# Optimization experiments

Measured on AMD Instinct MI355X. Metric: run time of the kernel, lower is better.

## Reference

```python
import jax, jax.numpy as jnp
import numpy as np

B, T, D, H, Dh, DF, MH = 4, 1024, 1024, 16, 64, 4096, 256
EPS = 1e-6


def setup_inputs() -> dict:
    key = jax.random.key(0)
    ks = jax.random.split(key, 10)
    s = 0.02
    w = lambda k, shape: jax.random.normal(k, shape, jnp.float32) * s
    return {
        "x": jax.random.normal(ks[0], (B, T, D), jnp.float32),
        "norm1_w": jnp.ones((D,), jnp.float32),
        "norm2_w": jnp.ones((D,), jnp.float32),
        "wq": w(ks[1], (D, D)),
        "wk": w(ks[2], (D, D)),
        "wv": w(ks[3], (D, D)),
        "wo": w(ks[4], (D, D)),
        "mnet_w1": w(ks[5], (D, MH)),
        "mnet_w2": w(ks[6], (MH, H * Dh)),
        "gate_w": w(ks[7], (D, DF)),
        "up_w": w(ks[8], (D, DF)),
        "down_w": w(ks[9], (DF, D)),
    }


def _rmsnorm(x, w):
    rms = jnp.sqrt(jnp.mean(x * x, axis=-1, keepdims=True) + EPS)
    return w * (x / rms)


def reference(x, norm1_w, norm2_w, wq, wk, wv, wo, mnet_w1, mnet_w2, gate_w, up_w, down_w):
    # --- pre-norm geodesic (DRM) attention ---
    h = _rmsnorm(x, norm1_w)  # [B,T,D]
    q = (h @ wq).reshape(B, T, H, Dh)
    k = (h @ wk).reshape(B, T, H, Dh)
    v = (h @ wv).reshape(B, T, H, Dh)
    # MetricNet: positive diagonal metric G(x) per token/head
    g = jax.nn.softplus(jax.nn.silu(h @ mnet_w1) @ mnet_w2).reshape(B, T, H, Dh)
    # squared geodesic distance under key-side diagonal metric, expanded form:
    # dist_ij = sum_d g_jd*(q_id - k_jd)^2 = q^2.g - 2 q.(g*k) + sum(g*k^2)
    gk = g * k
    dist = (
        jnp.einsum("bihd,bjhd->bhij", q * q, g)
        - 2.0 * jnp.einsum("bihd,bjhd->bhij", q, gk)
        + jnp.transpose(jnp.sum(gk * k, axis=-1), (0, 2, 1))[:, :, None, :]
    )  # [B,H,T,T]
    scores = -dist / np.float32(np.sqrt(Dh))
    causal = jnp.tril(jnp.ones((T, T), bool))
    scores = jnp.where(causal, scores, jnp.float32(-1e30))
    attn = jax.nn.softmax(scores, axis=-1)
    o = jnp.einsum("bhij,bjhd->bihd", attn, v).reshape(B, T, D) @ wo
    x = x + o
    # --- pre-norm SwiGLU FFN ---
    h2 = _rmsnorm(x, norm2_w)
    ffn = (jax.nn.silu(h2 @ gate_w) * (h2 @ up_w)) @ down_w
    return x + ffn
```

## Files before the change

### kernel.cpp

```cpp
#include <hip/hip_runtime.h>
#include <hip/hip_bf16.h>
#include <math.h>

#define BB  4
#define TT  1024
#define DD  1024
#define HH  16
#define DH  64
#define DFF 4096
#define MHH 256

typedef __attribute__((ext_vector_type(8))) short bf16x8;
typedef __attribute__((ext_vector_type(4))) float f32x4;
typedef unsigned int u32;

#define NEG_BIG (-1e9f)

__device__ __forceinline__ float b2f(short s) {
    union { unsigned int u; float f; } x;
    x.u = ((unsigned int)(unsigned short)s) << 16;
    return x.f;
}
__device__ __forceinline__ short f2b(float f) {
    union { float f; unsigned int u; } x; x.f = f;
    unsigned int r = x.u + 0x7fffu + ((x.u >> 16) & 1u);
    return (short)(r >> 16);
}
__device__ __forceinline__ float silu_f(float x) { return x / (1.f + __expf(-x)); }

__device__ __forceinline__ void gld16(const short* g, short* l) {
    __builtin_amdgcn_global_load_lds(
        (const __attribute__((address_space(1))) u32*)g,
        (__attribute__((address_space(3))) u32*)l, 16, 0, 0);
}

#define STAGE64(ga0, ga1, lds, kb)                                  \
    {                                                               \
        gld16((ga0) + (kb),      &(lds)[tid * 8]);                  \
        gld16((ga1) + (kb),      &(lds)[2048 + tid * 8]);           \
        gld16((ga0) + (kb) + 32, &(lds)[4096 + tid * 8]);           \
        gld16((ga1) + (kb) + 32, &(lds)[4096 + 2048 + tid * 8]);    \
    }

__device__ __forceinline__ void convT_tile_body(
    const float* __restrict__ src, short* __restrict__ dst,
    int K, int N, int bx, int by, int tid, short (*Ts)[36])
{
    const int k0 = by * 32, n0 = bx * 32;
    const int r = tid >> 3, c4 = (tid & 7) * 4;
    float4 v = *(const float4*)(src + (size_t)(k0 + r) * N + n0 + c4);
    Ts[r][c4 + 0] = f2b(v.x); Ts[r][c4 + 1] = f2b(v.y);
    Ts[r][c4 + 2] = f2b(v.z); Ts[r][c4 + 3] = f2b(v.w);
    __syncthreads();
    short4 o;
    o.x = Ts[c4 + 0][r]; o.y = Ts[c4 + 1][r];
    o.z = Ts[c4 + 2][r]; o.w = Ts[c4 + 3][r];
    *(short4*)(dst + (size_t)(n0 + r) * K + k0 + c4) = o;
}

__device__ __forceinline__ void rms_body(
    const float* __restrict__ X, const float* __restrict__ W,
    short* __restrict__ O, float* __restrict__ XC, int row, int tid, float* red)
{
    float4 xv = ((const float4*)(X + (size_t)row * DD))[tid];
    if (XC) ((float4*)(XC + (size_t)row * DD))[tid] = xv;
    float f0 = xv.x, f1 = xv.y, f2 = xv.z, f3 = xv.w;
    float ss = f0*f0 + f1*f1 + f2*f2 + f3*f3;
    #pragma unroll
    for (int m = 1; m < 64; m <<= 1) ss += __shfl_xor(ss, m);
    if ((tid & 63) == 0) red[tid >> 6] = ss;
    __syncthreads();
    float tot = red[0] + red[1] + red[2] + red[3];
    float scale = rsqrtf(tot * (1.f / DD) + 1e-6f);
    float4 wv = ((const float4*)W)[tid];
    short4 ov;
    ov.x = f2b(f0 * scale * wv.x);
    ov.y = f2b(f1 * scale * wv.y);
    ov.z = f2b(f2 * scale * wv.z);
    ov.w = f2b(f3 * scale * wv.w);
    ((short4*)(O + (size_t)row * DD))[tid] = ov;
}

__global__ __launch_bounds__(256) void pre_k(
    const float* __restrict__ wq, const float* __restrict__ wk,
    const float* __restrict__ wv, const float* __restrict__ mw1,
    const float* __restrict__ wo, const float* __restrict__ mw2,
    short* __restrict__ WfT, short* __restrict__ woT, short* __restrict__ mw2T,
    const float* __restrict__ x, const float* __restrict__ n1w,
    short* __restrict__ h, float* __restrict__ out)
{
    __shared__ __align__(16) short Ts[32][36];
    __shared__ float red[4];
    const int b = blockIdx.x, tid = threadIdx.x;
    if (b >= 4608) { rms_body(x, n1w, h, out, b - 4608, tid, red); return; }
    const float* src; short* dst; int K, N, bx, by;
    if (b < 1024)      { src = wq;  dst = WfT;               K = DD;  N = DD;  int l = b;        bx = l & 31; by = l >> 5; }
    else if (b < 2048) { src = wk;  dst = WfT + 1024 * 1024; K = DD;  N = DD;  int l = b - 1024; bx = l & 31; by = l >> 5; }
    else if (b < 3072) { src = wv;  dst = WfT + 2048 * 1024; K = DD;  N = DD;  int l = b - 2048; bx = l & 31; by = l >> 5; }
    else if (b < 3328) { src = mw1; dst = WfT + 3072 * 1024; K = DD;  N = MHH; int l = b - 3072; bx = l & 7;  by = l >> 3; }
    else if (b < 4352) { src = wo;  dst = woT;               K = DD;  N = DD;  int l = b - 3328; bx = l & 31; by = l >> 5; }
    else               { src = mw2; dst = mw2T;              K = MHH; N = DD;  int l = b - 4352; bx = l & 31; by = l >> 5; }
    convT_tile_body(src, dst, K, N, bx, by, tid, Ts);
}

__global__ __launch_bounds__(256) void ffn_k(
    const float* __restrict__ gw, const float* __restrict__ uw,
    const float* __restrict__ dw,
    short* __restrict__ WgT, short* __restrict__ WuT, short* __restrict__ WdT,
    const float* __restrict__ out, const float* __restrict__ n2w,
    short* __restrict__ h2)
{
    __shared__ __align__(16) short Ts[32][36];
    __shared__ float red[4];
    const int b = blockIdx.x, tid = threadIdx.x;
    if (b >= 12288) { rms_body(out, n2w, h2, nullptr, b - 12288, tid, red); return; }
    const float* src; short* dst; int K, N, bx, by;
    if (b < 4096)      { src = gw; dst = WgT; K = DD;  N = DFF; int l = b;        bx = l & 127; by = l >> 7; }
    else if (b < 8192) { src = uw; dst = WuT; K = DD;  N = DFF; int l = b - 4096; bx = l & 127; by = l >> 7; }
    else               { src = dw; dst = WdT; K = DFF; N = DD;  int l = b - 8192; bx = l & 31;  by = l >> 5; }
    convT_tile_body(src, dst, K, N, bx, by, tid, Ts);
}

#define EP_NONE     0
#define EP_SILU     1
#define EP_SOFTPLUS 2
#define EP_RES      3

template<int EP, bool CF32, bool AUXF32>
__global__ __launch_bounds__(256, 4) void gemm128_k(
    const short* __restrict__ A, const short* __restrict__ Bt,
    void* Cv, const void* auxv,
    int N, int K, int lda, int ldb)
{
    __shared__ __align__(16) short As[2 * 4096];
    __shared__ __align__(16) short Bs[2 * 4096];
    const int tid  = threadIdx.x;
    const int wave = tid >> 6, lane = tid & 63;
    const int l16  = lane & 15, quad = lane >> 4;
    const int m0 = blockIdx.y * 128, n0 = blockIdx.x * 128;
    const int wm = (wave & 1) * 64, wn = (wave >> 1) * 64;

    f32x4 acc[4][4];
    #pragma unroll
    for (int i = 0; i < 4; i++)
        #pragma unroll
        for (int j = 0; j < 4; j++) acc[i][j] = (f32x4){0.f, 0.f, 0.f, 0.f};

    const int srow = tid >> 2, scol = (tid & 3) * 8;
    const short* ga0 = A  + (size_t)(m0 + srow)      * lda + scol;
    const short* ga1 = A  + (size_t)(m0 + 64 + srow) * lda + scol;
    const short* gb0 = Bt + (size_t)(n0 + srow)      * ldb + scol;
    const short* gb1 = Bt + (size_t)(n0 + 64 + srow) * ldb + scol;

    for (int kb = 0; kb < K; kb += 64) {
        STAGE64(ga0, ga1, As, kb);
        STAGE64(gb0, gb1, Bs, kb);
        __syncthreads();
        #pragma unroll
        for (int kc = 0; kc < 2; kc++) {
            bf16x8 af[4], bf[4];
            #pragma unroll
            for (int mi = 0; mi < 4; mi++)
                af[mi] = *(bf16x8*)&As[kc * 4096 + (wm + mi * 16 + l16) * 32 + quad * 8];
            #pragma unroll
            for (int ni = 0; ni < 4; ni++)
                bf[ni] = *(bf16x8*)&Bs[kc * 4096 + (wn + ni * 16 + l16) * 32 + quad * 8];
            #pragma unroll
            for (int mi = 0; mi < 4; mi++)
                #pragma unroll
                for (int ni = 0; ni < 4; ni++)
                    acc[mi][ni] = __builtin_amdgcn_mfma_f32_16x16x32_bf16(af[mi], bf[ni], acc[mi][ni], 0, 0, 0);
        }
        __syncthreads();
    }
    #pragma unroll
    for (int mi = 0; mi < 4; mi++) {
        #pragma unroll
        for (int ni = 0; ni < 4; ni++) {
            #pragma unroll
            for (int r = 0; r < 4; r++) {
                int row = m0 + wm + mi * 16 + quad * 4 + r;
                int col = n0 + wn + ni * 16 + l16;
                size_t idx = (size_t)row * N + col;
                float v = acc[mi][ni][r];
                if (EP == EP_SILU)          v = silu_f(v);
                else if (EP == EP_SOFTPLUS) v = fmaxf(v, 0.f) + log1pf(__expf(-fabsf(v)));
                else if (EP == EP_RES) {
                    if (AUXF32) v += ((const float*)auxv)[idx];
                    else        v += b2f(((const short*)auxv)[idx]);
                }
                if (CF32) ((float*)Cv)[idx] = v;
                else      ((short*)Cv)[idx] = f2b(v);
            }
        }
    }
}

__global__ __launch_bounds__(256, 4) void gemm128_atomic_k(
    const short* __restrict__ A, const short* __restrict__ Bt,
    float* out, int N, int Kc, int lda, int ldb)
{
    __shared__ __align__(16) short As[2 * 4096];
    __shared__ __align__(16) short Bs[2 * 4096];
    const int tid  = threadIdx.x;
    const int wave = tid >> 6, lane = tid & 63;
    const int l16  = lane & 15, quad = lane >> 4;
    const int m0 = blockIdx.y * 128, n0 = blockIdx.x * 128;
    const int wm = (wave & 1) * 64, wn = (wave >> 1) * 64;
    const int koff = blockIdx.z * Kc;

    f32x4 acc[4][4];
    #pragma unroll
    for (int i = 0; i < 4; i++)
        #pragma unroll
        for (int j = 0; j < 4; j++) acc[i][j] = (f32x4){0.f, 0.f, 0.f, 0.f};

    const int srow = tid >> 2, scol = (tid & 3) * 8;
    const short* ga0 = A  + (size_t)(m0 + srow)      * lda + koff + scol;
    const short* ga1 = A  + (size_t)(m0 + 64 + srow) * lda + koff + scol;
    const short* gb0 = Bt + (size_t)(n0 + srow)      * ldb + koff + scol;
    const short* gb1 = Bt + (size_t)(n0 + 64 + srow) * ldb + koff + scol;

    for (int kb = 0; kb < Kc; kb += 64) {
        STAGE64(ga0, ga1, As, kb);
        STAGE64(gb0, gb1, Bs, kb);
        __syncthreads();
        #pragma unroll
        for (int kc = 0; kc < 2; kc++) {
            bf16x8 af[4], bf[4];
            #pragma unroll
            for (int mi = 0; mi < 4; mi++)
                af[mi] = *(bf16x8*)&As[kc * 4096 + (wm + mi * 16 + l16) * 32 + quad * 8];
            #pragma unroll
            for (int ni = 0; ni < 4; ni++)
                bf[ni] = *(bf16x8*)&Bs[kc * 4096 + (wn + ni * 16 + l16) * 32 + quad * 8];
            #pragma unroll
            for (int mi = 0; mi < 4; mi++)
                #pragma unroll
                for (int ni = 0; ni < 4; ni++)
                    acc[mi][ni] = __builtin_amdgcn_mfma_f32_16x16x32_bf16(af[mi], bf[ni], acc[mi][ni], 0, 0, 0);
        }
        __syncthreads();
    }
    #pragma unroll
    for (int mi = 0; mi < 4; mi++)
        #pragma unroll
        for (int ni = 0; ni < 4; ni++)
            #pragma unroll
            for (int r = 0; r < 4; r++) {
                int row = m0 + wm + mi * 16 + quad * 4 + r;
                int col = n0 + wn + ni * 16 + l16;
                atomicAdd(out + (size_t)row * N + col, acc[mi][ni][r]);
            }
}

__global__ __launch_bounds__(256, 4) void gemm128_qkvm_k(
    const short* __restrict__ A, const short* __restrict__ Wf,
    short* __restrict__ Qb, short* __restrict__ Kb, short* __restrict__ Vb,
    short* __restrict__ M1)
{
    __shared__ __align__(16) short As[2 * 4096];
    __shared__ __align__(16) short Bs[2 * 4096];
    const int tid  = threadIdx.x;
    const int wave = tid >> 6, lane = tid & 63;
    const int l16  = lane & 15, quad = lane >> 4;
    const int m0 = blockIdx.y * 128, n0 = blockIdx.x * 128;
    const int wm = (wave & 1) * 64, wn = (wave >> 1) * 64;
    const int K = DD;

    f32x4 acc[4][4];
    #pragma unroll
    for (int i = 0; i < 4; i++)
        #pragma unroll
        for (int j = 0; j < 4; j++) acc[i][j] = (f32x4){0.f, 0.f, 0.f, 0.f};

    const int srow = tid >> 2, scol = (tid & 3) * 8;
    const short* ga0 = A  + (size_t)(m0 + srow)      * K + scol;
    const short* ga1 = A  + (size_t)(m0 + 64 + srow) * K + scol;
    const short* gb0 = Wf + (size_t)(n0 + srow)      * K + scol;
    const short* gb1 = Wf + (size_t)(n0 + 64 + srow) * K + scol;

    for (int kb = 0; kb < K; kb += 64) {
        STAGE64(ga0, ga1, As, kb);
        STAGE64(gb0, gb1, Bs, kb);
        __syncthreads();
        #pragma unroll
        for (int kc = 0; kc < 2; kc++) {
            bf16x8 af[4], bf[4];
            #pragma unroll
            for (int mi = 0; mi < 4; mi++)
                af[mi] = *(bf16x8*)&As[kc * 4096 + (wm + mi * 16 + l16) * 32 + quad * 8];
            #pragma unroll
            for (int ni = 0; ni < 4; ni++)
                bf[ni] = *(bf16x8*)&Bs[kc * 4096 + (wn + ni * 16 + l16) * 32 + quad * 8];
            #pragma unroll
            for (int mi = 0; mi < 4; mi++)
                #pragma unroll
                for (int ni = 0; ni < 4; ni++)
                    acc[mi][ni] = __builtin_amdgcn_mfma_f32_16x16x32_bf16(af[mi], bf[ni], acc[mi][ni], 0, 0, 0);
        }
        __syncthreads();
    }
    short* dst; int base, ldc; bool dosilu = false;
    if      (n0 < 1024) { dst = Qb; base = 0;    ldc = 1024; }
    else if (n0 < 2048) { dst = Kb; base = 1024; ldc = 1024; }
    else if (n0 < 3072) { dst = Vb; base = 2048; ldc = 1024; }
    else                { dst = M1; base = 3072; ldc = 256; dosilu = true; }
    #pragma unroll
    for (int mi = 0; mi < 4; mi++)
        #pragma unroll
        for (int ni = 0; ni < 4; ni++)
            #pragma unroll
            for (int r = 0; r < 4; r++) {
                int row = m0 + wm + mi * 16 + quad * 4 + r;
                int col = n0 + wn + ni * 16 + l16 - base;
                float v = acc[mi][ni][r];
                if (dosilu) v = silu_f(v);
                dst[(size_t)row * ldc + col] = f2b(v);
            }
}

__global__ __launch_bounds__(256, 2) void gemm128_swiglu_k(
    const short* __restrict__ A, const short* __restrict__ Gt,
    const short* __restrict__ Ut, short* __restrict__ F,
    int N, int K, int ldb)
{
    __shared__ __align__(16) short As[2 * 4096];
    __shared__ __align__(16) short Gs[2 * 4096];
    __shared__ __align__(16) short Us[2 * 4096];
    const int tid  = threadIdx.x;
    const int wave = tid >> 6, lane = tid & 63;
    const int l16  = lane & 15, quad = lane >> 4;

    int bx = blockIdx.x, by = blockIdx.y;
    {
        const int gx = gridDim.x;
        if ((gx & 7) == 0) {
            const int orig = by * gx + bx;
            const int xcd = orig & 7, j = orig >> 3;
            const int xpx = gx >> 3;
            bx = xcd * xpx + (j % xpx);
            by = j / xpx;
        }
    }
    const int m0 = by * 128, n0 = bx * 128;
    const int wm = (wave & 1) * 64, wn = (wave >> 1) * 64;

    f32x4 ag[4][4], au[4][4];
    #pragma unroll
    for (int i = 0; i < 4; i++)
        #pragma unroll
        for (int j = 0; j < 4; j++) {
            ag[i][j] = (f32x4){0.f, 0.f, 0.f, 0.f};
            au[i][j] = (f32x4){0.f, 0.f, 0.f, 0.f};
        }

    const int srow = tid >> 2, scol = (tid & 3) * 8;
    const short* ga0 = A  + (size_t)(m0 + srow)      * K   + scol;
    const short* ga1 = A  + (size_t)(m0 + 64 + srow) * K   + scol;
    const short* gg0 = Gt + (size_t)(n0 + srow)      * ldb + scol;
    const short* gg1 = Gt + (size_t)(n0 + 64 + srow) * ldb + scol;
    const short* gu0 = Ut + (size_t)(n0 + srow)      * ldb + scol;
    const short* gu1 = Ut + (size_t)(n0 + 64 + srow) * ldb + scol;

    for (int kb = 0; kb < K; kb += 64) {
        STAGE64(ga0, ga1, As, kb);
        STAGE64(gg0, gg1, Gs, kb);
        STAGE64(gu0, gu1, Us, kb);
        __syncthreads();
        #pragma unroll
        for (int kc = 0; kc < 2; kc++) {
            bf16x8 af[4], gf[4], uf[4];
            #pragma unroll
            for (int mi = 0; mi < 4; mi++)
                af[mi] = *(bf16x8*)&As[kc * 4096 + (wm + mi * 16 + l16) * 32 + quad * 8];
            #pragma unroll
            for (int ni = 0; ni < 4; ni++) {
                gf[ni] = *(bf16x8*)&Gs[kc * 4096 + (wn + ni * 16 + l16) * 32 + quad * 8];
                uf[ni] = *(bf16x8*)&Us[kc * 4096 + (wn + ni * 16 + l16) * 32 + quad * 8];
            }
            #pragma unroll
            for (int mi = 0; mi < 4; mi++)
                #pragma unroll
                for (int ni = 0; ni < 4; ni++) {
                    ag[mi][ni] = __builtin_amdgcn_mfma_f32_16x16x32_bf16(af[mi], gf[ni], ag[mi][ni], 0, 0, 0);
                    au[mi][ni] = __builtin_amdgcn_mfma_f32_16x16x32_bf16(af[mi], uf[ni], au[mi][ni], 0, 0, 0);
                }
        }
        __syncthreads();
    }
    #pragma unroll
    for (int mi = 0; mi < 4; mi++)
        #pragma unroll
        for (int ni = 0; ni < 4; ni++)
            #pragma unroll
            for (int r = 0; r < 4; r++) {
                int row = m0 + wm + mi * 16 + quad * 4 + r;
                int col = n0 + wn + ni * 16 + l16;
                F[(size_t)row * N + col] = f2b(silu_f(ag[mi][ni][r]) * au[mi][ni][r]);
            }
}

__global__ __launch_bounds__(256) void gkc_k(
    const short* __restrict__ G, short* KG,
    float* __restrict__ Cj)
{
    const int bt  = blockIdx.x;
    const int tid = threadIdx.x;
    const int h = tid >> 4, d0 = (tid & 15) * 4;
    const size_t base = (size_t)bt * (HH * DH) + h * DH + d0;
    short4 gv = *(const short4*)(G + base);
    short4 kv = *(const short4*)(KG + base);
    float g0 = b2f(gv.x), g1 = b2f(gv.y), g2 = b2f(gv.z), g3 = b2f(gv.w);
    float k0 = b2f(kv.x), k1 = b2f(kv.y), k2 = b2f(kv.z), k3 = b2f(kv.w);
    float p0 = g0*k0, p1 = g1*k1, p2 = g2*k2, p3 = g3*k3;
    short4 ov; ov.x = f2b(p0); ov.y = f2b(p1); ov.z = f2b(p2); ov.w = f2b(p3);
    *(short4*)(KG + base) = ov;
    float cc = p0*k0 + p1*k1 + p2*k2 + p3*k3;
    #pragma unroll
    for (int m = 1; m < 16; m <<= 1) cc += __shfl_xor(cc, m);
    if ((tid & 15) == 0) {
        int b = bt >> 10, t = bt & (TT - 1);
        Cj[((size_t)b * HH + h) * TT + t] = cc;
    }
}

__global__ __launch_bounds__(256) void attn_k(
    const short* __restrict__ Q, const short* __restrict__ G,
    const short* __restrict__ GK, const short* __restrict__ V,
    const float* __restrict__ Cj, short* __restrict__ O)
{
    __shared__ __align__(16) short Gs[64][72];
    __shared__ __align__(16) short GKs[64][72];
    __shared__ __align__(16) short Vt[64][72];
    __shared__ __align__(16) float Cs[64];
    __shared__ __align__(16) short Ps[4][16][72];

    const int pair = blockIdx.x;
    const int bh = blockIdx.y;
    const int b = bh >> 4, h = bh & 15;
    const int tid  = threadIdx.x;
    const int wave = tid >> 6, lane = tid & 63;
    const int l16  = lane & 15, quad = lane >> 4;

    const size_t bh_base = ((size_t)b * TT) * (HH * DH) + (size_t)h * DH;
    const float* cj_row = Cj + ((size_t)b * HH + h) * TT;

    const int sr2 = tid >> 3, sc2 = (tid & 7) * 8;
    const f32x4 z = {0.f, 0.f, 0.f, 0.f};

    for (int halfsel = 0; halfsel < 2; halfsel++) {
        const int it = halfsel ? 15 - pair : pair;
        const int i0 = it * 64;

        const int qrow = i0 + wave * 16 + l16;
        bf16x8 qf[2], qqf[2];
        #pragma unroll
        for (int kc = 0; kc < 2; kc++) {
            qf[kc] = *(const bf16x8*)(Q + bh_base + (size_t)qrow * (HH * DH) + kc * 32 + quad * 8);
            #pragma unroll
            for (int j = 0; j < 8; j++) {
                float f = b2f(qf[kc][j]);
                qqf[kc][j] = f2b(f * f);
            }
        }

        float m_i[4], l_i[4];
        f32x4 o_acc[4] = {z, z, z, z};
        #pragma unroll
        for (int r = 0; r < 4; r++) { m_i[r] = NEG_BIG; l_i[r] = 0.f; }

        for (int jt = 0; jt <= it; jt++) {
            const int j0 = jt * 64;
            #pragma unroll
            for (int pass = 0; pass < 2; pass++) {
                int jr = sr2 + pass * 32;
                size_t rb = bh_base + (size_t)(j0 + jr) * (HH * DH) + sc2;
                *(int4*)&Gs[jr][sc2]  = *(const int4*)(G + rb);
                *(int4*)&GKs[jr][sc2] = *(const int4*)(GK + rb);
                int4 vvec = *(const int4*)(V + rb);
                const short* vv = (const short*)&vvec;
                #pragma unroll
                for (int jj = 0; jj < 8; jj++) Vt[sc2 + jj][jr] = vv[jj];
            }
            if (tid < 64) Cs[tid] = cj_row[j0 + tid];
            __syncthreads();

            f32x4 s1[4] = {z, z, z, z}, s2[4] = {z, z, z, z};
            #pragma unroll
            for (int ns = 0; ns < 4; ns++) {
                #pragma unroll
                for (int kc = 0; kc < 2; kc++) {
                    bf16x8 gf  = *(bf16x8*)&Gs [ns * 16 + l16][kc * 32 + quad * 8];
                    bf16x8 gkf = *(bf16x8*)&GKs[ns * 16 + l16][kc * 32 + quad * 8];
                    s1[ns] = __builtin_amdgcn_mfma_f32_16x16x32_bf16(qqf[kc], gf,  s1[ns], 0, 0, 0);
                    s2[ns] = __builtin_amdgcn_mfma_f32_16x16x32_bf16(qf[kc],  gkf, s2[ns], 0, 0, 0);
                }
            }

            float p[4][4];
            #pragma unroll
            for (int ns = 0; ns < 4; ns++) {
                float cjv = Cs[ns * 16 + l16];
                #pragma unroll
                for (int r = 0; r < 4; r++)
                    p[ns][r] = (2.f * s2[ns][r] - s1[ns][r] - cjv) * 0.125f;
            }
            if (jt == it) {
                #pragma unroll
                for (int ns = 0; ns < 4; ns++) {
                    int j = j0 + ns * 16 + l16;
                    #pragma unroll
                    for (int r = 0; r < 4; r++) {
                        int i = i0 + wave * 16 + quad * 4 + r;
                        if (j > i) p[ns][r] = NEG_BIG;
                    }
                }
            }

            #pragma unroll
            for (int r = 0; r < 4; r++) {
                float mx = fmaxf(fmaxf(p[0][r], p[1][r]), fmaxf(p[2][r], p[3][r]));
                #pragma unroll
                for (int d2 = 1; d2 < 16; d2 <<= 1) mx = fmaxf(mx, __shfl_xor(mx, d2));
                float mnew = fmaxf(m_i[r], mx);
                float corr = __expf(m_i[r] - mnew);
                float sp = 0.f;
                #pragma unroll
                for (int ns = 0; ns < 4; ns++) {
                    float e = __expf(p[ns][r] - mnew);
                    p[ns][r] = e; sp += e;
                }
                #pragma unroll
                for (int d2 = 1; d2 < 16; d2 <<= 1) sp += __shfl_xor(sp, d2);
                l_i[r] = l_i[r] * corr + sp;
                m_i[r] = mnew;
                #pragma unroll
                for (int nv = 0; nv < 4; nv++) o_acc[nv][r] *= corr;
            }

            #pragma unroll
            for (int ns = 0; ns < 4; ns++)
                #pragma unroll
                for (int r = 0; r < 4; r++)
                    Ps[wave][quad * 4 + r][ns * 16 + l16] = f2b(p[ns][r]);

            bf16x8 pf[2];
            pf[0] = *(bf16x8*)&Ps[wave][l16][quad * 8];
            pf[1] = *(bf16x8*)&Ps[wave][l16][32 + quad * 8];
            #pragma unroll
            for (int nv = 0; nv < 4; nv++) {
                #pragma unroll
                for (int kc = 0; kc < 2; kc++) {
                    bf16x8 vf = *(bf16x8*)&Vt[nv * 16 + l16][kc * 32 + quad * 8];
                    o_acc[nv] = __builtin_amdgcn_mfma_f32_16x16x32_bf16(pf[kc], vf, o_acc[nv], 0, 0, 0);
                }
            }
            __syncthreads();
        }

        #pragma unroll
        for (int nv = 0; nv < 4; nv++) {
            #pragma unroll
            for (int r = 0; r < 4; r++) {
                int i = i0 + wave * 16 + quad * 4 + r;
                int d = nv * 16 + l16;
                O[bh_base + (size_t)i * (HH * DH) + d] = f2b(o_acc[nv][r] / l_i[r]);
            }
        }
    }
}

extern "C" void kernel_launch(void* const* d_in, const int* in_sizes, int n_in,
                              void* d_out, int out_size, void* d_ws, size_t ws_size,
                              hipStream_t stream)
{
    const float* x   = (const float*)d_in[0];
    const float* n1w = (const float*)d_in[1];
    const float* n2w = (const float*)d_in[2];
    const float* wq  = (const float*)d_in[3];
    const float* wk  = (const float*)d_in[4];
    const float* wv  = (const float*)d_in[5];
    const float* wo  = (const float*)d_in[6];
    const float* mw1 = (const float*)d_in[7];
    const float* mw2 = (const float*)d_in[8];
    const float* gw  = (const float*)d_in[9];
    const float* uw  = (const float*)d_in[10];
    const float* dw  = (const float*)d_in[11];
    float* out = (float*)d_out;

    const size_t MB = 1u << 20;
    if (ws_size < 48 * MB) return;
    const bool bigF = (ws_size >= 64 * MB);
    char* wsb = (char*)d_ws;
    short* h    = (short*)(wsb);
    short* g    = (short*)(wsb);
    short* h2   = (short*)(wsb);
    short* qb   = (short*)(wsb + 8 * MB);
    short* WgT  = (short*)(wsb + 8 * MB);
    short* kb   = (short*)(wsb + 16 * MB);
    short* WuT  = (short*)(wsb + 16 * MB);
    short* vb   = (short*)(wsb + 24 * MB);
    short* WdT  = (short*)(wsb + 24 * MB);
    short* WfT  = (short*)(wsb + 32 * MB);
    short* ob   = (short*)(wsb + 32 * MB);
    short* F    = (short*)(wsb + 32 * MB);
    short* woT  = (short*)(wsb + 40 * MB);
    short* m1   = (short*)(wsb + 42 * MB);
    float* cj   = (float*)(wsb + 44 * MB);
    short* mw2T = (short*)(wsb + 44 * MB + 512 * 1024);

    const int M = BB * TT;

    pre_k<<<4608 + M, 256, 0, stream>>>(wq, wk, wv, mw1, wo, mw2,
                                        WfT, woT, mw2T, x, n1w, h, out);

    gemm128_qkvm_k<<<dim3(3328 / 128, M / 128), 256, 0, stream>>>(h, WfT, qb, kb, vb, m1);
    gemm128_k<EP_SOFTPLUS,false,false><<<dim3(DD / 128, M / 128), 256, 0, stream>>>(
        m1, mw2T, g, nullptr, DD, MHH, MHH, MHH);
    gkc_k<<<M, 256, 0, stream>>>(g, kb, cj);
    attn_k<<<dim3(8, BB * HH), 256, 0, stream>>>(qb, g, kb, vb, cj, ob);

    gemm128_atomic_k<<<dim3(DD / 128, M / 128, 2), 256, 0, stream>>>(
        ob, woT, out, DD, 512, DD, DD);

    ffn_k<<<12288 + M, 256, 0, stream>>>(gw, uw, dw, WgT, WuT, WdT, out, n2w, h2);

    if (bigF) {
        gemm128_swiglu_k<<<dim3(DFF / 128, M / 128), 256, 0, stream>>>(h2, WgT, WuT, F, DFF, DD, DD);
        gemm128_atomic_k<<<dim3(DD / 128, M / 128, 2), 256, 0, stream>>>(
            F, WdT, out, DD, 2048, DFF, DFF);
    } else {
        const int NH = DFF / 2;
        for (int half = 0; half < 2; half++) {
            gemm128_swiglu_k<<<dim3(NH / 128, M / 128), 256, 0, stream>>>(
                h2, WgT + (size_t)half * NH * DD, WuT + (size_t)half * NH * DD, F, NH, DD, DD);
            gemm128_atomic_k<<<dim3(DD / 128, M / 128, 2), 256, 0, stream>>>(
                F, WdT + (size_t)half * NH, out, DD, 1024, NH, DFF);
        }
    }
}
```

Baseline: 461.3 us.

## Fuse softplus metric GEMM with g*k product and row-sum; swizzle V tile in LDS

The separate gkc_k pass is folded into the MetricNet second GEMM epilogue. The epilogue now computes softplus, writes G, overwrites K with g*k in place, and reduces sum(g*k^2) per head through lane shuffles, which removes one kernel launch and a full reread of G and K. Separately, the transposed V tile in LDS in the attention kernel gets an XOR swizzle on column index to reduce bank conflicts on the transposing writes and the MFMA fragment reads. The swizzle must stay consistent between the write and read index formulas.

```diff
diff --git a/kernel.cpp b/kernel.cpp
--- a/kernel.cpp
+++ b/kernel.cpp
@@ -121,81 +121,6 @@
     convT_tile_body(src, dst, K, N, bx, by, tid, Ts);
 }
 
-#define EP_NONE     0
-#define EP_SILU     1
-#define EP_SOFTPLUS 2
-#define EP_RES      3
-
-template<int EP, bool CF32, bool AUXF32>
-__global__ __launch_bounds__(256, 4) void gemm128_k(
-    const short* __restrict__ A, const short* __restrict__ Bt,
-    void* Cv, const void* auxv,
-    int N, int K, int lda, int ldb)
-{
-    __shared__ __align__(16) short As[2 * 4096];
-    __shared__ __align__(16) short Bs[2 * 4096];
-    const int tid  = threadIdx.x;
-    const int wave = tid >> 6, lane = tid & 63;
-    const int l16  = lane & 15, quad = lane >> 4;
-    const int m0 = blockIdx.y * 128, n0 = blockIdx.x * 128;
-    const int wm = (wave & 1) * 64, wn = (wave >> 1) * 64;
-
-    f32x4 acc[4][4];
-    #pragma unroll
-    for (int i = 0; i < 4; i++)
-        #pragma unroll
-        for (int j = 0; j < 4; j++) acc[i][j] = (f32x4){0.f, 0.f, 0.f, 0.f};
-
-    const int srow = tid >> 2, scol = (tid & 3) * 8;
-    const short* ga0 = A  + (size_t)(m0 + srow)      * lda + scol;
-    const short* ga1 = A  + (size_t)(m0 + 64 + srow) * lda + scol;
-    const short* gb0 = Bt + (size_t)(n0 + srow)      * ldb + scol;
-    const short* gb1 = Bt + (size_t)(n0 + 64 + srow) * ldb + scol;
-
-    for (int kb = 0; kb < K; kb += 64) {
-        STAGE64(ga0, ga1, As, kb);
-        STAGE64(gb0, gb1, Bs, kb);
-        __syncthreads();
-        #pragma unroll
-        for (int kc = 0; kc < 2; kc++) {
-            bf16x8 af[4], bf[4];
-            #pragma unroll
-            for (int mi = 0; mi < 4; mi++)
-                af[mi] = *(bf16x8*)&As[kc * 4096 + (wm + mi * 16 + l16) * 32 + quad * 8];
-            #pragma unroll
-            for (int ni = 0; ni < 4; ni++)
-                bf[ni] = *(bf16x8*)&Bs[kc * 4096 + (wn + ni * 16 + l16) * 32 + quad * 8];
-            #pragma unroll
-            for (int mi = 0; mi < 4; mi++)
-                #pragma unroll
-                for (int ni = 0; ni < 4; ni++)
-                    acc[mi][ni] = __builtin_amdgcn_mfma_f32_16x16x32_bf16(af[mi], bf[ni], acc[mi][ni], 0, 0, 0);
-        }
-        __syncthreads();
-    }
-    #pragma unroll
-    for (int mi = 0; mi < 4; mi++) {
-        #pragma unroll
-        for (int ni = 0; ni < 4; ni++) {
-            #pragma unroll
-            for (int r = 0; r < 4; r++) {
-                int row = m0 + wm + mi * 16 + quad * 4 + r;
-                int col = n0 + wn + ni * 16 + l16;
-                size_t idx = (size_t)row * N + col;
-                float v = acc[mi][ni][r];
-                if (EP == EP_SILU)          v = silu_f(v);
-                else if (EP == EP_SOFTPLUS) v = fmaxf(v, 0.f) + log1pf(__expf(-fabsf(v)));
-                else if (EP == EP_RES) {
-                    if (AUXF32) v += ((const float*)auxv)[idx];
-                    else        v += b2f(((const short*)auxv)[idx]);
-                }
-                if (CF32) ((float*)Cv)[idx] = v;
-                else      ((short*)Cv)[idx] = f2b(v);
-            }
-        }
-    }
-}
-
 __global__ __launch_bounds__(256, 4) void gemm128_atomic_k(
     const short* __restrict__ A, const short* __restrict__ Bt,
     float* out, int N, int Kc, int lda, int ldb)
@@ -318,6 +243,83 @@
                 if (dosilu) v = silu_f(v);
                 dst[(size_t)row * ldc + col] = f2b(v);
             }
+}
+
+__global__ __launch_bounds__(256, 4) void gemm128_mnet2_k(
+    const short* __restrict__ A, const short* __restrict__ Bt,
+    short* __restrict__ G, short* KG, float* __restrict__ Cj)
+{
+    __shared__ __align__(16) short As[2 * 4096];
+    __shared__ __align__(16) short Bs[2 * 4096];
+    const int tid  = threadIdx.x;
+    const int wave = tid >> 6, lane = tid & 63;
+    const int l16  = lane & 15, quad = lane >> 4;
+    const int m0 = blockIdx.y * 128, n0 = blockIdx.x * 128;
+    const int wm = (wave & 1) * 64, wn = (wave >> 1) * 64;
+    const int K = MHH;
+
+    f32x4 acc[4][4];
+    #pragma unroll
+    for (int i = 0; i < 4; i++)
+        #pragma unroll
+        for (int j = 0; j < 4; j++) acc[i][j] = (f32x4){0.f, 0.f, 0.f, 0.f};
+
+    const int srow = tid >> 2, scol = (tid & 3) * 8;
+    const short* ga0 = A  + (size_t)(m0 + srow)      * K + scol;
+    const short* ga1 = A  + (size_t)(m0 + 64 + srow) * K + scol;
+    const short* gb0 = Bt + (size_t)(n0 + srow)      * K + scol;
+    const short* gb1 = Bt + (size_t)(n0 + 64 + srow) * K + scol;
+
+    for (int kk = 0; kk < K; kk += 64) {
+        STAGE64(ga0, ga1, As, kk);
+        STAGE64(gb0, gb1, Bs, kk);
+        __syncthreads();
+        #pragma unroll
+        for (int kc = 0; kc < 2; kc++) {
+            bf16x8 af[4], bf[4];
+            #pragma unroll
+            for (int mi = 0; mi < 4; mi++)
+                af[mi] = *(bf16x8*)&As[kc * 4096 + (wm + mi * 16 + l16) * 32 + quad * 8];
+            #pragma unroll
+            for (int ni = 0; ni < 4; ni++)
+                bf[ni] = *(bf16x8*)&Bs[kc * 4096 + (wn + ni * 16 + l16) * 32 + quad * 8];
+            #pragma unroll
+            for (int mi = 0; mi < 4; mi++)
+                #pragma unroll
+                for (int ni = 0; ni < 4; ni++)
+                    acc[mi][ni] = __builtin_amdgcn_mfma_f32_16x16x32_bf16(af[mi], bf[ni], acc[mi][ni], 0, 0, 0);
+        }
+        __syncthreads();
+    }
+    const int hidx = (n0 + wn) >> 6;
+    #pragma unroll
+    for (int mi = 0; mi < 4; mi++) {
+        #pragma unroll
+        for (int r = 0; r < 4; r++) {
+            const int row = m0 + wm + mi * 16 + quad * 4 + r;
+            float ccv = 0.f;
+            #pragma unroll
+            for (int ni = 0; ni < 4; ni++) {
+                const int col = n0 + wn + ni * 16 + l16;
+                const size_t idx = (size_t)row * DD + col;
+                float v = acc[mi][ni][r];
+                v = fmaxf(v, 0.f) + log1pf(__expf(-fabsf(v)));
+                short gb = f2b(v);
+                G[idx] = gb;
+                float gf = b2f(gb);
+                float kf = b2f(KG[idx]);
+                float p  = gf * kf;
+                KG[idx] = f2b(p);
+                ccv += p * kf;
+            }
+            #pragma unroll
+            for (int m = 1; m < 16; m <<= 1) ccv += __shfl_xor(ccv, m);
+            if (l16 == 0) {
+                int bidx = row >> 10, t = row & (TT - 1);
+                Cj[((size_t)bidx * HH + hidx) * TT + t] = ccv;
+            }
+        }
+    }
 }
 
 __global__ __launch_bounds__(256, 2) void gemm128_swiglu_k(
@@ -401,30 +403,6 @@
             }
 }
 
-__global__ __launch_bounds__(256) void gkc_k(
-    const short* __restrict__ G, short* KG,
-    float* __restrict__ Cj)
-{
-    const int bt  = blockIdx.x;
-    const int tid = threadIdx.x;
-    const int h = tid >> 4, d0 = (tid & 15) * 4;
-    const size_t base = (size_t)bt * (HH * DH) + h * DH + d0;
-    short4 gv = *(const short4*)(G + base);
-    short4 kv = *(const short4*)(KG + base);
-    float g0 = b2f(gv.x), g1 = b2f(gv.y), g2 = b2f(gv.z), g3 = b2f(gv.w);
-    float k0 = b2f(kv.x), k1 = b2f(kv.y), k2 = b2f(kv.z), k3 = b2f(kv.w);
-    float p0 = g0*k0, p1 = g1*k1, p2 = g2*k2, p3 = g3*k3;
-    short4 ov; ov.x = f2b(p0); ov.y = f2b(p1); ov.z = f2b(p2); ov.w = f2b(p3);
-    *(short4*)(KG + base) = ov;
-    float cc = p0*k0 + p1*k1 + p2*k2 + p3*k3;
-    #pragma unroll
-    for (int m = 1; m < 16; m <<= 1) cc += __shfl_xor(cc, m);
-    if ((tid & 15) == 0) {
-        int b = bt >> 10, t = bt & (TT - 1);
-        Cj[((size_t)b * HH + h) * TT + t] = cc;
-    }
-}
-
 __global__ __launch_bounds__(256) void attn_k(
     const short* __restrict__ Q, const short* __restrict__ G,
     const short* __restrict__ GK, const short* __restrict__ V,
@@ -447,6 +425,7 @@
     const float* cj_row = Cj + ((size_t)b * HH + h) * TT;
 
     const int sr2 = tid >> 3, sc2 = (tid & 7) * 8;
+    const int vswz = (tid & 7) << 3;
     const f32x4 z = {0.f, 0.f, 0.f, 0.f};
 
     for (int halfsel = 0; halfsel < 2; halfsel++) {
@@ -481,7 +460,7 @@
                 int4 vvec = *(const int4*)(V + rb);
                 const short* vv = (const short*)&vvec;
                 #pragma unroll
-                for (int jj = 0; jj < 8; jj++) Vt[sc2 + jj][jr] = vv[jj];
+                for (int jj = 0; jj < 8; jj++) Vt[sc2 + jj][jr ^ vswz] = vv[jj];
             }
             if (tid < 64) Cs[tid] = cj_row[j0 + tid];
             __syncthreads();
@@ -550,9 +529,10 @@
             pf[1] = *(bf16x8*)&Ps[wave][l16][32 + quad * 8];
             #pragma unroll
             for (int nv = 0; nv < 4; nv++) {
+                const int vx = ((2 * nv + (l16 >> 3)) & 7) << 3;
                 #pragma unroll
                 for (int kc = 0; kc < 2; kc++) {
-                    bf16x8 vf = *(bf16x8*)&Vt[nv * 16 + l16][kc * 32 + quad * 8];
+                    bf16x8 vf = *(bf16x8*)&Vt[nv * 16 + l16][(kc * 32 + quad * 8) ^ vx];
                     o_acc[nv] = __builtin_amdgcn_mfma_f32_16x16x32_bf16(pf[kc], vf, o_acc[nv], 0, 0, 0);
                 }
             }
@@ -616,9 +596,9 @@
                                         WfT, woT, mw2T, x, n1w, h, out);
 
     gemm128_qkvm_k<<<dim3(3328 / 128, M / 128), 256, 0, stream>>>(h, WfT, qb, kb, vb, m1);
-    gemm128_k<EP_SOFTPLUS,false,false><<<dim3(DD / 128, M / 128), 256, 0, stream>>>(
-        m1, mw2T, g, nullptr, DD, MHH, MHH, MHH);
-    gkc_k<<<M, 256, 0, stream>>>(g, kb, cj);
+
+    gemm128_mnet2_k<<<dim3(DD / 128, M / 128), 256, 0, stream>>>(m1, mw2T, g, kb, cj);
+
     attn_k<<<dim3(8, BB * HH), 256, 0, stream>>>(qb, g, kb, vb, cj, ob);
 
     gemm128_atomic_k<<<dim3(DD / 128, M / 128, 2), 256, 0, stream>>>(
```

Measured after the change: 585.1 us. 26.8% more time.
